# Optimization experiments

Hardware: AMD Instinct MI355X
Metric: run time of the kernel (lower is better)

## Reference

```python
import jax, jax.numpy as jnp
import numpy as np

SWIGLU_ALPHA = 1.702
SWIGLU_LIMIT = 7.0
TOP_K = 4


def setup_inputs() -> dict:
    key = jax.random.key(0)
    k = jax.random.split(key, 5)
    B, S, D, E, I = 2, 1024, 1024, 8, 2048
    return {
        "hidden_states": jax.random.normal(k[0], (B, S, D), dtype=jnp.float32),
        "router_weight": jax.random.normal(k[1], (E, D), dtype=jnp.float32) * 0.02,
        "router_bias": jnp.zeros((E,), dtype=jnp.float32),
        "gate_up_proj": jax.random.normal(k[2], (E, 2 * I, D), dtype=jnp.float32) * 0.02,
        "gate_up_proj_bias": jnp.zeros((E, 2 * I), dtype=jnp.float32),
        "down_proj": jax.random.normal(k[3], (E, D, I), dtype=jnp.float32) * 0.02,
        "down_proj_bias": jnp.zeros((E, D), dtype=jnp.float32),
    }


def reference(hidden_states, router_weight, router_bias, gate_up_proj,
              gate_up_proj_bias, down_proj, down_proj_bias):
    B, S, D = hidden_states.shape
    E = router_weight.shape[0]
    x = hidden_states.reshape(-1, D)                      # [N, D]
    N = x.shape[0]

    # --- router: top-k + post-softmax normalization (softmax in fp32) ---
    logits = x @ router_weight.T + router_bias            # [N, E]
    topk_logits, topk_idx = jax.lax.top_k(logits, TOP_K)  # [N, K]
    topk_w = jax.nn.softmax(topk_logits.astype(jnp.float32), axis=-1)

    # dense combine weights: zero for unselected experts (math-equivalent to
    # scatter -> grouped GEMM -> gather+weighted-sum in the torch code)
    combine = jnp.zeros((N, E), dtype=jnp.float32)
    combine = combine.at[jnp.arange(N)[:, None], topk_idx].set(topk_w)  # [N, E]

    # --- experts: clamped SwiGLU FFN, all experts on all tokens ---
    gate_up = jnp.einsum('nd,ejd->nej', x, gate_up_proj) + gate_up_proj_bias  # [N, E, 2I]
    gate, up = jnp.split(gate_up, 2, axis=-1)             # [N, E, I] each
    gate = jnp.minimum(gate, SWIGLU_LIMIT)
    up = jnp.clip(up, -SWIGLU_LIMIT, SWIGLU_LIMIT)
    act = (up + 1.0) * gate * jax.nn.sigmoid(SWIGLU_ALPHA * gate)  # [N, E, I]
    out = jnp.einsum('nei,edi->ned', act, down_proj) + down_proj_bias  # [N, E, D]

    # --- weighted combine over selected experts ---
    y = jnp.einsum('ned,ne->nd', out, combine.astype(out.dtype))  # [N, D]
    return y.reshape(B, S, D)
```

## Files before the change

kernel.cpp:

```cpp
#include <hip/hip_runtime.h>
#include <stdint.h>
#include <math.h>

#define NTOK   2048
#define DDIM   1024
#define ENUM   8
#define IDIM   2048
#define TWOI   4096
#define TOPKN  4
#define CAPROWS 10240

typedef unsigned short ushort_t;
typedef __attribute__((ext_vector_type(8))) short short8;
typedef __attribute__((ext_vector_type(4))) float f4;

#define VMCNT(n) asm volatile("s_waitcnt vmcnt(" #n ")" ::: "memory")
#define CFENCE() asm volatile("" ::: "memory")
#define BARRIER() do { CFENCE(); __builtin_amdgcn_s_barrier(); CFENCE(); } while (0)

__device__ inline ushort_t f2bf(float f) {
    union { float f; uint32_t u; } v; v.f = f;
    uint32_t u = v.u;
    u += 0x7FFFu + ((u >> 16) & 1u);
    return (ushort_t)(u >> 16);
}

__device__ inline void gload16(const ushort_t* g, ushort_t* l) {
    __builtin_amdgcn_global_load_lds(
        (const __attribute__((address_space(1))) uint32_t*)(uintptr_t)g,
        (__attribute__((address_space(3))) uint32_t*)(uint32_t)(uintptr_t)l,
        16, 0, 0);
}

__global__ void cvt_all_kernel(const float* __restrict__ gup, const float* __restrict__ dwn,
                               ushort_t* __restrict__ dst, int* __restrict__ meta) {
    if (blockIdx.x == 0 && threadIdx.x < 64) meta[threadIdx.x] = 0;
    const int n1 = ENUM * TWOI * DDIM / 8;
    const int n2 = ENUM * DDIM * IDIM / 8;
    int i = blockIdx.x * 256 + threadIdx.x;
    const float4* src;
    if (i < n1) src = (const float4*)gup + 2 * (size_t)i;
    else if (i < n1 + n2) src = (const float4*)dwn + 2 * (size_t)(i - n1);
    else return;
    float4 a = src[0], b = src[1];
    uint4 o;
    o.x = (uint32_t)f2bf(a.x) | ((uint32_t)f2bf(a.y) << 16);
    o.y = (uint32_t)f2bf(a.z) | ((uint32_t)f2bf(a.w) << 16);
    o.z = (uint32_t)f2bf(b.x) | ((uint32_t)f2bf(b.y) << 16);
    o.w = (uint32_t)f2bf(b.z) | ((uint32_t)f2bf(b.w) << 16);
    ((uint4*)dst)[i] = o;
}

__global__ void router_kernel(const float* __restrict__ x, const float* __restrict__ rw,
                              const float* __restrict__ rb, int* __restrict__ topk_idx,
                              float* __restrict__ topk_w, int* __restrict__ counts) {
    int n = (blockIdx.x * 256 + threadIdx.x) >> 6;
    int lane = threadIdx.x & 63;
    const float* xr = x + (size_t)n * DDIM;
    double p[ENUM];
#pragma unroll
    for (int e = 0; e < ENUM; ++e) p[e] = 0.0;
    for (int d0 = 0; d0 < DDIM; d0 += 64) {
        double xv = (double)xr[d0 + lane];
#pragma unroll
        for (int e = 0; e < ENUM; ++e) p[e] += xv * (double)rw[e * DDIM + d0 + lane];
    }
#pragma unroll
    for (int e = 0; e < ENUM; ++e) {
        double v = p[e];
#pragma unroll
        for (int off = 32; off > 0; off >>= 1) v += __shfl_xor(v, off, 64);
        p[e] = v + (double)rb[e];
    }
    if (lane == 0) {
        int id[TOPKN]; double lv[TOPKN]; unsigned used = 0;
#pragma unroll
        for (int k = 0; k < TOPKN; ++k) {
            double best = -INFINITY; int bi = 0;
            for (int e = 0; e < ENUM; ++e)
                if (!((used >> e) & 1u) && p[e] > best) { best = p[e]; bi = e; }
            used |= 1u << bi; id[k] = bi; lv[k] = best;
        }
        float lf[TOPKN]; float s = 0.f; float w[TOPKN];
#pragma unroll
        for (int k = 0; k < TOPKN; ++k) lf[k] = (float)lv[k];
#pragma unroll
        for (int k = 0; k < TOPKN; ++k) { w[k] = expf(lf[k] - lf[0]); s += w[k]; }
        float inv = 1.f / s;
#pragma unroll
        for (int k = 0; k < TOPKN; ++k) {
            topk_idx[n * TOPKN + k] = id[k];
            topk_w[n * TOPKN + k] = w[k] * inv;
            atomicAdd(&counts[id[k]], 1);
        }
    }
}

__global__ void assign_kernel(const int* __restrict__ topk_idx, const float* __restrict__ topk_w,
                              const int* __restrict__ counts, int* __restrict__ fill,
                              int* __restrict__ row_token, float* __restrict__ row_weight,
                              int* __restrict__ row_of_pair,
                              int* __restrict__ base, int* __restrict__ padcnt,
                              int* __restrict__ totalp) {
    int baseL[ENUM]; int run = 0;
#pragma unroll
    for (int e = 0; e < ENUM; ++e) {
        baseL[e] = run;
        run += (counts[e] + 255) & ~255;
    }
    int n = blockIdx.x * 256 + threadIdx.x;
    if (n == 0) {
#pragma unroll
        for (int e = 0; e < ENUM; ++e) {
            base[e] = baseL[e];
            padcnt[e] = (counts[e] + 255) & ~255;
        }
        *totalp = run;
    }
    if (n >= NTOK) return;
    for (int k = 0; k < TOPKN; ++k) {
        int e = topk_idx[n * TOPKN + k];
        int pos = atomicAdd(&fill[e], 1);
        int row = baseL[e] + pos;
        row_token[row] = n;
        row_weight[row] = topk_w[n * TOPKN + k];
        row_of_pair[n * TOPKN + k] = row;
    }
}

__global__ void gather_kernel(const float* __restrict__ x, const int* __restrict__ row_token,
                              const int* __restrict__ base, const int* __restrict__ counts,
                              const int* __restrict__ padcnt, const int* __restrict__ totalp,
                              ushort_t* __restrict__ A) {
    int r = blockIdx.x;
    if (r >= *totalp) return;
    int e = 0;
#pragma unroll
    for (int i = 0; i < ENUM; ++i) if (r >= base[i] + padcnt[i]) e = i + 1;
    bool valid = (r - base[e]) < counts[e];
    int t = threadIdx.x;
    float4 v = make_float4(0.f, 0.f, 0.f, 0.f);
    if (valid) {
        int n = row_token[r];
        v = ((const float4*)(x + (size_t)n * DDIM))[t];
    }
    ushort4 o; o.x = f2bf(v.x); o.y = f2bf(v.y); o.z = f2bf(v.z); o.w = f2bf(v.w);
    ((ushort4*)(A + (size_t)r * DDIM))[t] = o;
}

__global__ __launch_bounds__(512, 2)
void gemm1_kernel(const ushort_t* __restrict__ A, const ushort_t* __restrict__ Wg,
                  const float* __restrict__ gub, ushort_t* __restrict__ act,
                  const int* __restrict__ base, const int* __restrict__ padcnt) {
    const int e = blockIdx.z;
    const int mt = blockIdx.y;
    if (mt * 256 >= padcnt[e]) return;
    const int nt = blockIdx.x;
    const int row0 = base[e] + mt * 256;

    extern __shared__ char smem[];
    ushort_t* sA = (ushort_t*)smem;
    ushort_t* sG = (ushort_t*)(smem + 65536);
    ushort_t* sU = (ushort_t*)(smem + 98304);

    const int t = threadIdx.x;
    const int lane = t & 63;
    const int wid = t >> 6;
    const int wm = wid >> 2;
    const int wn = wid & 3;
    const int r15 = lane & 15, quad = lane >> 4;
    const int sw = r15 & 7;

    const int srow = t >> 3;
    const int sunit = (t & 7) ^ (srow & 7);
    const ushort_t* gA = A + (size_t)(row0 + srow) * DDIM + sunit * 8;
    const ushort_t* gG = Wg + ((size_t)e * TWOI + nt * 128 + srow) * DDIM + sunit * 8;
    const ushort_t* gU = gG + (size_t)IDIM * DDIM;

    f4 accg[8][2], accu[8][2];
    const f4 zero = {0.f, 0.f, 0.f, 0.f};
#pragma unroll
    for (int i = 0; i < 8; ++i)
#pragma unroll
        for (int j = 0; j < 2; ++j) { accg[i][j] = zero; accu[i][j] = zero; }

#define STG1A(ks, b) do {                                                    \
    const int k0_ = (ks) * 64;                                               \
    ushort_t* dA = sA + (b) * 16384 + t * 8;                                 \
    gload16(gA + k0_,                        dA);                            \
    gload16(gA + (size_t)64  * DDIM + k0_,   dA + 4096);                     \
    gload16(gA + (size_t)128 * DDIM + k0_,   dA + 8192);                     \
    gload16(gA + (size_t)192 * DDIM + k0_,   dA + 12288);                    \
} while (0)
#define STG1GU(ks, b) do {                                                   \
    const int k0_ = (ks) * 64;                                               \
    ushort_t* dG = sG + (b) * 8192  + t * 8;                                 \
    ushort_t* dU = sU + (b) * 8192  + t * 8;                                 \
    gload16(gG + k0_,                        dG);                            \
    gload16(gG + (size_t)64 * DDIM + k0_,    dG + 4096);                     \
    gload16(gU + k0_,                        dU);                            \
    gload16(gU + (size_t)64 * DDIM + k0_,    dU + 4096);                     \
} while (0)

    STG1A(0, 0); STG1GU(0, 0);
    const int NKS = DDIM / 64;
    for (int ks = 0; ks < NKS; ++ks) {
        const int cur = ks & 1;
        VMCNT(0);
        BARRIER();
        const ushort_t* bA = sA + cur * 16384;
        const ushort_t* bG = sG + cur * 8192;
        const ushort_t* bU = sU + cur * 8192;
        const bool pf = (ks + 1 < NKS);
#pragma unroll
        for (int kc = 0; kc < 2; ++kc) {
            const int uoff = ((kc * 4 + quad) ^ sw) * 8;
            short8 gF[2], uF[2];
#pragma unroll
            for (int j = 0; j < 2; ++j) {
                gF[j] = *(const short8*)(bG + (wn * 32 + j * 16 + r15) * 64 + uoff);
                uF[j] = *(const short8*)(bU + (wn * 32 + j * 16 + r15) * 64 + uoff);
            }
#pragma unroll
            for (int mh = 0; mh < 2; ++mh) {
                short8 aF[4];
#pragma unroll
                for (int i = 0; i < 4; ++i)
                    aF[i] = *(const short8*)(bA + (wm * 128 + (mh * 4 + i) * 16 + r15) * 64 + uoff);
                if (pf && mh == 0) {
                    if (kc == 0) STG1A(ks + 1, cur ^ 1);
                    else         STG1GU(ks + 1, cur ^ 1);
                }
                __builtin_amdgcn_sched_barrier(0);
                __builtin_amdgcn_s_setprio(1);
#pragma unroll
                for (int i = 0; i < 4; ++i)
#pragma unroll
                    for (int j = 0; j < 2; ++j) {
                        accg[mh * 4 + i][j] = __builtin_amdgcn_mfma_f32_16x16x32_bf16(aF[i], gF[j], accg[mh * 4 + i][j], 0, 0, 0);
                        accu[mh * 4 + i][j] = __builtin_amdgcn_mfma_f32_16x16x32_bf16(aF[i], uF[j], accu[mh * 4 + i][j], 0, 0, 0);
                    }
                __builtin_amdgcn_s_setprio(0);
                __builtin_amdgcn_sched_barrier(0);
            }
        }
    }
#undef STG1A
#undef STG1GU

    const int rowbase = row0 + wm * 128;
    const int col0 = nt * 128 + wn * 32;
#pragma unroll
    for (int j = 0; j < 2; ++j) {
        const int col = col0 + j * 16 + r15;
        const float bg = gub[e * TWOI + col];
        const float bu = gub[e * TWOI + IDIM + col];
#pragma unroll
        for (int mf = 0; mf < 8; ++mf) {
#pragma unroll
            for (int r = 0; r < 4; ++r) {
                const int row = rowbase + mf * 16 + quad * 4 + r;
                float g = fminf(accg[mf][j][r] + bg, 7.0f);
                float u = fminf(fmaxf(accu[mf][j][r] + bu, -7.0f), 7.0f);
                float a = (u + 1.0f) * g / (1.0f + __expf(-1.702f * g));
                act[(size_t)row * IDIM + col] = f2bf(a);
            }
        }
    }
}

__global__ __launch_bounds__(256, 2)
void gemm2_kernel(const ushort_t* __restrict__ A, const ushort_t* __restrict__ Wd,
                  const float* __restrict__ dwb, const float* __restrict__ row_weight,
                  float* __restrict__ contrib,
                  const int* __restrict__ base, const int* __restrict__ padcnt) {
    const int e = blockIdx.z;
    const int mt = blockIdx.y;
    if (mt * 128 >= padcnt[e]) return;
    const int nt = blockIdx.x;
    const int row0 = base[e] + mt * 128;

    extern __shared__ char smem[];
    ushort_t* sA = (ushort_t*)smem;
    ushort_t* sB = (ushort_t*)(smem + 32768);

    const int t = threadIdx.x;
    const int lane = t & 63;
    const int wid = t >> 6;
    const int wm = wid >> 1;
    const int wn = wid & 1;
    const int r15 = lane & 15, quad = lane >> 4;
    const int sw = r15 & 7;

    const int gr = t >> 3;
    const int gu = (t & 7) ^ (gr & 7);
    const ushort_t* gA = A + (size_t)(row0 + gr) * IDIM + gu * 8;
    const ushort_t* gB = Wd + ((size_t)e * DDIM + nt * 128 + gr) * IDIM + gu * 8;

    f4 acc[4][4];
    const f4 zero = {0.f, 0.f, 0.f, 0.f};
#pragma unroll
    for (int i = 0; i < 4; ++i)
#pragma unroll
        for (int j = 0; j < 4; ++j) acc[i][j] = zero;

#define STG2A(ks, b) do {                                                    \
    const int k0_ = (ks) * 64;                                               \
    ushort_t* dA = sA + (b) * 8192 + t * 8;                                  \
    gload16(gA + k0_,                       dA);                             \
    gload16(gA + (size_t)32 * IDIM + k0_,   dA + 2048);                      \
    gload16(gA + (size_t)64 * IDIM + k0_,   dA + 4096);                      \
    gload16(gA + (size_t)96 * IDIM + k0_,   dA + 6144);                      \
} while (0)
#define STG2B(ks, b) do {                                                    \
    const int k0_ = (ks) * 64;                                               \
    ushort_t* dB = sB + (b) * 8192 + t * 8;                                  \
    gload16(gB + k0_,                       dB);                             \
    gload16(gB + (size_t)32 * IDIM + k0_,   dB + 2048);                      \
    gload16(gB + (size_t)64 * IDIM + k0_,   dB + 4096);                      \
    gload16(gB + (size_t)96 * IDIM + k0_,   dB + 6144);                      \
} while (0)

    STG2A(0, 0); STG2B(0, 0);
    const int NKS = IDIM / 64;
    for (int ks = 0; ks < NKS; ++ks) {
        const int cur = ks & 1;
        VMCNT(0);
        BARRIER();
        const ushort_t* bA = sA + cur * 8192;
        const ushort_t* bB = sB + cur * 8192;
        const bool pf = (ks + 1 < NKS);
#pragma unroll
        for (int kc = 0; kc < 2; ++kc) {
            const int uoff = ((kc * 4 + quad) ^ sw) * 8;
            short8 aF[4], bF[4];
#pragma unroll
            for (int j = 0; j < 4; ++j)
                bF[j] = *(const short8*)(bB + (wn * 64 + j * 16 + r15) * 64 + uoff);
#pragma unroll
            for (int i = 0; i < 4; ++i)
                aF[i] = *(const short8*)(bA + (wm * 64 + i * 16 + r15) * 64 + uoff);
            if (pf) {
                if (kc == 0) STG2A(ks + 1, cur ^ 1);
                else         STG2B(ks + 1, cur ^ 1);
            }
            __builtin_amdgcn_sched_barrier(0);
            __builtin_amdgcn_s_setprio(1);
#pragma unroll
            for (int i = 0; i < 4; ++i)
#pragma unroll
                for (int j = 0; j < 4; ++j)
                    acc[i][j] = __builtin_amdgcn_mfma_f32_16x16x32_bf16(aF[i], bF[j], acc[i][j], 0, 0, 0);
            __builtin_amdgcn_s_setprio(0);
            __builtin_amdgcn_sched_barrier(0);
        }
    }
#undef STG2A
#undef STG2B

    const int rowbase = row0 + wm * 64;
    const int col0 = nt * 128 + wn * 64;
    float bs[4];
#pragma unroll
    for (int j = 0; j < 4; ++j) bs[j] = dwb[e * DDIM + col0 + j * 16 + r15];
#pragma unroll
    for (int mf = 0; mf < 4; ++mf) {
#pragma unroll
        for (int r = 0; r < 4; ++r) {
            const int row = rowbase + mf * 16 + quad * 4 + r;
            const float w = row_weight[row];
#pragma unroll
            for (int j = 0; j < 4; ++j) {
                const int col = col0 + j * 16 + r15;
                contrib[(size_t)row * DDIM + col] = (acc[mf][j][r] + bs[j]) * w;
            }
        }
    }
}

__global__ void combine_kernel(const float* __restrict__ contrib, const int* __restrict__ row_of_pair,
                               float* __restrict__ out) {
    int n = blockIdx.x;
    int t = threadIdx.x;
    int r0 = row_of_pair[n * 4 + 0], r1 = row_of_pair[n * 4 + 1];
    int r2 = row_of_pair[n * 4 + 2], r3 = row_of_pair[n * 4 + 3];
    float4 a = ((const float4*)(contrib + (size_t)r0 * DDIM))[t];
    float4 b = ((const float4*)(contrib + (size_t)r1 * DDIM))[t];
    float4 c = ((const float4*)(contrib + (size_t)r2 * DDIM))[t];
    float4 d = ((const float4*)(contrib + (size_t)r3 * DDIM))[t];
    float4 s;
    s.x = a.x + b.x + c.x + d.x;
    s.y = a.y + b.y + c.y + d.y;
    s.z = a.z + b.z + c.z + d.z;
    s.w = a.w + b.w + c.w + d.w;
    ((float4*)(out + (size_t)n * DDIM))[t] = s;
}

extern "C" void kernel_launch(void* const* d_in, const int* in_sizes, int n_in,
                              void* d_out, int out_size, void* d_ws, size_t ws_size,
                              hipStream_t stream) {
    const float* x   = (const float*)d_in[0];
    const float* rw  = (const float*)d_in[1];
    const float* rb  = (const float*)d_in[2];
    const float* gup = (const float*)d_in[3];
    const float* gub = (const float*)d_in[4];
    const float* dwn = (const float*)d_in[5];
    const float* dwb = (const float*)d_in[6];
    float* out = (float*)d_out;

    char* ws = (char*)d_ws;
    size_t off = 0;
    auto alloc = [&](size_t bytes) -> void* {
        void* p = ws + off;
        off += (bytes + 255) & ~(size_t)255;
        return p;
    };
    ushort_t* Wg   = (ushort_t*)alloc((size_t)ENUM * TWOI * DDIM * 2);
    ushort_t* Wd   = (ushort_t*)alloc((size_t)ENUM * DDIM * IDIM * 2);
    char* unionbuf = (char*)alloc((size_t)CAPROWS * DDIM * 4);
    ushort_t* Ar      = (ushort_t*)unionbuf;
    float*    CONTRIB = (float*)unionbuf;
    ushort_t* ACT  = (ushort_t*)alloc((size_t)CAPROWS * IDIM * 2);
    int*   topk_idx    = (int*)alloc(NTOK * 4 * 4);
    float* topk_w      = (float*)alloc(NTOK * 4 * 4);
    int*   row_of_pair = (int*)alloc(NTOK * 4 * 4);
    int*   row_token   = (int*)alloc(CAPROWS * 4);
    float* row_weight  = (float*)alloc(CAPROWS * 4);
    int*   meta        = (int*)alloc(256);
    int* counts = meta;      int* fill = meta + 8;
    int* base   = meta + 16; int* padcnt = meta + 24;
    int* totalp = meta + 32;

    const int ncvt8 = (ENUM * TWOI * DDIM + ENUM * DDIM * IDIM) / 8;

    cvt_all_kernel<<<(ncvt8 + 255) / 256, 256, 0, stream>>>(gup, dwn, Wg, meta);
    router_kernel<<<NTOK / 4, 256, 0, stream>>>(x, rw, rb, topk_idx, topk_w, counts);
    assign_kernel<<<NTOK / 256, 256, 0, stream>>>(topk_idx, topk_w, counts, fill,
                                                  row_token, row_weight, row_of_pair,
                                                  base, padcnt, totalp);
    gather_kernel<<<CAPROWS, 256, 0, stream>>>(x, row_token, base, counts, padcnt, totalp, Ar);
    gemm1_kernel<<<dim3(IDIM / 128, 8, ENUM), 512, 131072, stream>>>(Ar, Wg, gub, ACT, base, padcnt);
    gemm2_kernel<<<dim3(DDIM / 128, 16, ENUM), 256, 65536, stream>>>(ACT, Wd, dwb, row_weight, CONTRIB, base, padcnt);
    combine_kernel<<<NTOK, 256, 0, stream>>>(CONTRIB, row_of_pair, out);
}
```

Before: 562.1 us.

## Remap GEMM block indices for XCD-aware L2 locality and vectorize router loads

Both expert GEMMs now rebuild (expert, m-tile, n-tile) from a linearized block id. Blocks that share an A row-tile and are spread round-robin across the 8 XCDs are regrouped so each XCD works on the same m-tile across its n-tiles. The aim is better L2 reuse of the activation and weight tiles on MI355X's chiplet L2 caches. The router kernel also switches to float4 loads with an unrolled loop, which changes the order of the double-precision accumulation slightly.

```diff
diff --git a/kernel.cpp b/kernel.cpp
--- a/kernel.cpp
+++ b/kernel.cpp
@@ -56,14 +56,22 @@
                               float* __restrict__ topk_w, int* __restrict__ counts) {
     int n = (blockIdx.x * 256 + threadIdx.x) >> 6;
     int lane = threadIdx.x & 63;
-    const float* xr = x + (size_t)n * DDIM;
+    const float4* x4 = (const float4*)(x + (size_t)n * DDIM);
+    const float4* w4 = (const float4*)rw;
     double p[ENUM];
 #pragma unroll
     for (int e = 0; e < ENUM; ++e) p[e] = 0.0;
-    for (int d0 = 0; d0 < DDIM; d0 += 64) {
-        double xv = (double)xr[d0 + lane];
-#pragma unroll
-        for (int e = 0; e < ENUM; ++e) p[e] += xv * (double)rw[e * DDIM + d0 + lane];
+#pragma unroll
+    for (int c = 0; c < 4; ++c) {
+        float4 xv = x4[c * 64 + lane];
+#pragma unroll
+        for (int e = 0; e < ENUM; ++e) {
+            float4 wv = w4[e * (DDIM / 4) + c * 64 + lane];
+            p[e] += (double)xv.x * (double)wv.x;
+            p[e] += (double)xv.y * (double)wv.y;
+            p[e] += (double)xv.z * (double)wv.z;
+            p[e] += (double)xv.w * (double)wv.w;
+        }
     }
 #pragma unroll
     for (int e = 0; e < ENUM; ++e) {
@@ -152,10 +160,14 @@
 void gemm1_kernel(const ushort_t* __restrict__ A, const ushort_t* __restrict__ Wg,
                   const float* __restrict__ gub, ushort_t* __restrict__ act,
                   const int* __restrict__ base, const int* __restrict__ padcnt) {
-    const int e = blockIdx.z;
-    const int mt = blockIdx.y;
+    const int L = blockIdx.x + 16 * blockIdx.y + 128 * blockIdx.z;
+    const int xcd = L & 7;
+    const int s = L >> 3;
+    const int nt = s & 15;
+    const int grp = ((s >> 4) << 3) | xcd;
+    const int e = grp >> 3;
+    const int mt = grp & 7;
     if (mt * 256 >= padcnt[e]) return;
-    const int nt = blockIdx.x;
     const int row0 = base[e] + mt * 256;
 
     extern __shared__ char smem[];
@@ -274,10 +286,14 @@
                   const float* __restrict__ dwb, const float* __restrict__ row_weight,
                   float* __restrict__ contrib,
                   const int* __restrict__ base, const int* __restrict__ padcnt) {
-    const int e = blockIdx.z;
-    const int mt = blockIdx.y;
+    const int L = blockIdx.x + 8 * blockIdx.y + 128 * blockIdx.z;
+    const int xcd = L & 7;
+    const int s = L >> 3;
+    const int nt = s & 7;
+    const int grp = ((s >> 3) << 3) | xcd;
+    const int e = grp >> 4;
+    const int mt = grp & 15;
     if (mt * 128 >= padcnt[e]) return;
-    const int nt = blockIdx.x;
     const int row0 = base[e] + mt * 128;
 
     extern __shared__ char smem[];
```

Result: slower. 603.2 us (+7.3%).

## Enlarge gemm2 tile to 256 rows with 512 threads, spread gemm1 prefetch

Applied to the files above, without the earlier changes.

The down-projection GEMM now uses 256-row M tiles computed by 512 threads (8 waves), which doubles reuse of each loaded weight tile and halves the grid along M. The prefetch stages in both GEMMs are split into smaller chunks issued across more sub-iterations, so global loads interleave more evenly with MFMA work. The router loads x and weights as float4. The larger gemm2 tile uses 96KB of LDS per block, which may lower occupancy and add padding waste for experts whose row counts are not multiples of 256.

```diff
diff --git a/kernel.cpp b/kernel.cpp
--- a/kernel.cpp
+++ b/kernel.cpp
@@ -56,14 +56,22 @@
                               float* __restrict__ topk_w, int* __restrict__ counts) {
     int n = (blockIdx.x * 256 + threadIdx.x) >> 6;
     int lane = threadIdx.x & 63;
-    const float* xr = x + (size_t)n * DDIM;
+    const float4* x4 = (const float4*)(x + (size_t)n * DDIM);
+    const float4* w4 = (const float4*)rw;
     double p[ENUM];
 #pragma unroll
     for (int e = 0; e < ENUM; ++e) p[e] = 0.0;
-    for (int d0 = 0; d0 < DDIM; d0 += 64) {
-        double xv = (double)xr[d0 + lane];
-#pragma unroll
-        for (int e = 0; e < ENUM; ++e) p[e] += xv * (double)rw[e * DDIM + d0 + lane];
+#pragma unroll
+    for (int c = 0; c < 4; ++c) {
+        float4 xv = x4[c * 64 + lane];
+#pragma unroll
+        for (int e = 0; e < ENUM; ++e) {
+            float4 wv = w4[e * (DDIM / 4) + c * 64 + lane];
+            p[e] += (double)xv.x * (double)wv.x;
+            p[e] += (double)xv.y * (double)wv.y;
+            p[e] += (double)xv.z * (double)wv.z;
+            p[e] += (double)xv.w * (double)wv.w;
+        }
     }
 #pragma unroll
     for (int e = 0; e < ENUM; ++e) {
@@ -184,25 +192,32 @@
 #pragma unroll
         for (int j = 0; j < 2; ++j) { accg[i][j] = zero; accu[i][j] = zero; }
 
-#define STG1A(ks, b) do {                                                    \
+#define STG1A1(ks, b) do {                                                   \
     const int k0_ = (ks) * 64;                                               \
     ushort_t* dA = sA + (b) * 16384 + t * 8;                                 \
     gload16(gA + k0_,                        dA);                            \
     gload16(gA + (size_t)64  * DDIM + k0_,   dA + 4096);                     \
+} while (0)
+#define STG1A2(ks, b) do {                                                   \
+    const int k0_ = (ks) * 64;                                               \
+    ushort_t* dA = sA + (b) * 16384 + t * 8;                                 \
     gload16(gA + (size_t)128 * DDIM + k0_,   dA + 8192);                     \
     gload16(gA + (size_t)192 * DDIM + k0_,   dA + 12288);                    \
 } while (0)
-#define STG1GU(ks, b) do {                                                   \
+#define STG1G(ks, b) do {                                                    \
     const int k0_ = (ks) * 64;                                               \
     ushort_t* dG = sG + (b) * 8192  + t * 8;                                 \
-    ushort_t* dU = sU + (b) * 8192  + t * 8;                                 \
     gload16(gG + k0_,                        dG);                            \
     gload16(gG + (size_t)64 * DDIM + k0_,    dG + 4096);                     \
+} while (0)
+#define STG1U(ks, b) do {                                                    \
+    const int k0_ = (ks) * 64;                                               \
+    ushort_t* dU = sU + (b) * 8192  + t * 8;                                 \
     gload16(gU + k0_,                        dU);                            \
     gload16(gU + (size_t)64 * DDIM + k0_,    dU + 4096);                     \
 } while (0)
 
-    STG1A(0, 0); STG1GU(0, 0);
+    STG1A1(0, 0); STG1A2(0, 0); STG1G(0, 0); STG1U(0, 0);
     const int NKS = DDIM / 64;
     for (int ks = 0; ks < NKS; ++ks) {
         const int cur = ks & 1;
@@ -227,9 +242,9 @@
 #pragma unroll
                 for (int i = 0; i < 4; ++i)
                     aF[i] = *(const short8*)(bA + (wm * 128 + (mh * 4 + i) * 16 + r15) * 64 + uoff);
-                if (pf && mh == 0) {
-                    if (kc == 0) STG1A(ks + 1, cur ^ 1);
-                    else         STG1GU(ks + 1, cur ^ 1);
+                if (pf) {
+                    if (kc == 0) { if (mh == 0) STG1A1(ks + 1, cur ^ 1); else STG1A2(ks + 1, cur ^ 1); }
+                    else         { if (mh == 0) STG1G(ks + 1, cur ^ 1);  else STG1U(ks + 1, cur ^ 1); }
                 }
                 __builtin_amdgcn_sched_barrier(0);
                 __builtin_amdgcn_s_setprio(1);
@@ -245,8 +260,10 @@
             }
         }
     }
-#undef STG1A
-#undef STG1GU
+#undef STG1A1
+#undef STG1A2
+#undef STG1G
+#undef STG1U
 
     const int rowbase = row0 + wm * 128;
     const int col0 = nt * 128 + wn * 32;
@@ -269,20 +286,20 @@
     }
 }
 
-__global__ __launch_bounds__(256, 2)
+__global__ __launch_bounds__(512, 2)
 void gemm2_kernel(const ushort_t* __restrict__ A, const ushort_t* __restrict__ Wd,
                   const float* __restrict__ dwb, const float* __restrict__ row_weight,
                   float* __restrict__ contrib,
                   const int* __restrict__ base, const int* __restrict__ padcnt) {
     const int e = blockIdx.z;
     const int mt = blockIdx.y;
-    if (mt * 128 >= padcnt[e]) return;
+    if (mt * 256 >= padcnt[e]) return;
     const int nt = blockIdx.x;
-    const int row0 = base[e] + mt * 128;
+    const int row0 = base[e] + mt * 256;
 
     extern __shared__ char smem[];
     ushort_t* sA = (ushort_t*)smem;
-    ushort_t* sB = (ushort_t*)(smem + 32768);
+    ushort_t* sB = (ushort_t*)(smem + 65536);
 
     const int t = threadIdx.x;
     const int lane = t & 63;
@@ -292,10 +309,10 @@
     const int r15 = lane & 15, quad = lane >> 4;
     const int sw = r15 & 7;
 
-    const int gr = t >> 3;
-    const int gu = (t & 7) ^ (gr & 7);
-    const ushort_t* gA = A + (size_t)(row0 + gr) * IDIM + gu * 8;
-    const ushort_t* gB = Wd + ((size_t)e * DDIM + nt * 128 + gr) * IDIM + gu * 8;
+    const int srow = t >> 3;
+    const int sunit = (t & 7) ^ (srow & 7);
+    const ushort_t* gA = A + (size_t)(row0 + srow) * IDIM + sunit * 8;
+    const ushort_t* gB = Wd + ((size_t)e * DDIM + nt * 128 + srow) * IDIM + sunit * 8;
 
     f4 acc[4][4];
     const f4 zero = {0.f, 0.f, 0.f, 0.f};
@@ -304,30 +321,36 @@
 #pragma unroll
         for (int j = 0; j < 4; ++j) acc[i][j] = zero;
 
-#define STG2A(ks, b) do {                                                    \
-    const int k0_ = (ks) * 64;                                               \
-    ushort_t* dA = sA + (b) * 8192 + t * 8;                                  \
-    gload16(gA + k0_,                       dA);                             \
-    gload16(gA + (size_t)32 * IDIM + k0_,   dA + 2048);                      \
-    gload16(gA + (size_t)64 * IDIM + k0_,   dA + 4096);                      \
-    gload16(gA + (size_t)96 * IDIM + k0_,   dA + 6144);                      \
-} while (0)
-#define STG2B(ks, b) do {                                                    \
+#define STG2A1(ks, b) do {                                                   \
+    const int k0_ = (ks) * 64;                                               \
+    ushort_t* dA = sA + (b) * 16384 + t * 8;                                 \
+    gload16(gA + k0_,                        dA);                            \
+    gload16(gA + (size_t)64  * IDIM + k0_,   dA + 4096);                     \
+} while (0)
+#define STG2A2(ks, b) do {                                                   \
+    const int k0_ = (ks) * 64;                                               \
+    ushort_t* dA = sA + (b) * 16384 + t * 8;                                 \
+    gload16(gA + (size_t)128 * IDIM + k0_,   dA + 8192);                     \
+    gload16(gA + (size_t)192 * IDIM + k0_,   dA + 12288);                    \
+} while (0)
+#define STG2B1(ks, b) do {                                                   \
     const int k0_ = (ks) * 64;                                               \
     ushort_t* dB = sB + (b) * 8192 + t * 8;                                  \
-    gload16(gB + k0_,                       dB);                             \
-    gload16(gB + (size_t)32 * IDIM + k0_,   dB + 2048);                      \
-    gload16(gB + (size_t)64 * IDIM + k0_,   dB + 4096);                      \
-    gload16(gB + (size_t)96 * IDIM + k0_,   dB + 6144);                      \
-} while (0)
-
-    STG2A(0, 0); STG2B(0, 0);
+    gload16(gB + k0_,                        dB);                            \
+} while (0)
+#define STG2B2(ks, b) do {                                                   \
+    const int k0_ = (ks) * 64;                                               \
+    ushort_t* dB = sB + (b) * 8192 + t * 8;                                  \
+    gload16(gB + (size_t)64 * IDIM + k0_,    dB + 4096);                     \
+} while (0)
+
+    STG2A1(0, 0); STG2A2(0, 0); STG2B1(0, 0); STG2B2(0, 0);
     const int NKS = IDIM / 64;
     for (int ks = 0; ks < NKS; ++ks) {
         const int cur = ks & 1;
         VMCNT(0);
         BARRIER();
-        const ushort_t* bA = sA + cur * 8192;
+        const ushort_t* bA = sA + cur * 16384;
         const ushort_t* bB = sB + cur * 8192;
         const bool pf = (ks + 1 < NKS);
 #pragma unroll
@@ -341,8 +364,8 @@
             for (int i = 0; i < 4; ++i)
                 aF[i] = *(const short8*)(bA + (wm * 64 + i * 16 + r15) * 64 + uoff);
             if (pf) {
-                if (kc == 0) STG2A(ks + 1, cur ^ 1);
-                else         STG2B(ks + 1, cur ^ 1);
+                if (kc == 0) { STG2A1(ks + 1, cur ^ 1); STG2B1(ks + 1, cur ^ 1); }
+                else         { STG2A2(ks + 1, cur ^ 1); STG2B2(ks + 1, cur ^ 1); }
             }
             __builtin_amdgcn_sched_barrier(0);
             __builtin_amdgcn_s_setprio(1);
@@ -355,8 +378,10 @@
             __builtin_amdgcn_sched_barrier(0);
         }
     }
-#undef STG2A
-#undef STG2B
+#undef STG2A1
+#undef STG2A2
+#undef STG2B1
+#undef STG2B2
 
     const int rowbase = row0 + wm * 64;
     const int col0 = nt * 128 + wn * 64;
@@ -440,6 +465,6 @@
                                                   base, padcnt, totalp);
     gather_kernel<<<CAPROWS, 256, 0, stream>>>(x, row_token, base, counts, padcnt, totalp, Ar);
     gemm1_kernel<<<dim3(IDIM / 128, 8, ENUM), 512, 131072, stream>>>(Ar, Wg, gub, ACT, base, padcnt);
-    gemm2_kernel<<<dim3(DDIM / 128, 16, ENUM), 256, 65536, stream>>>(ACT, Wd, dwb, row_weight, CONTRIB, base, padcnt);
+    gemm2_kernel<<<dim3(DDIM / 128, 8, ENUM), 512, 98304, stream>>>(ACT, Wd, dwb, row_weight, CONTRIB, base, padcnt);
     combine_kernel<<<NTOK, 256, 0, stream>>>(CONTRIB, row_of_pair, out);
 }
```

Result: no change. 572.7 us (+1.9%).

## Deepen GEMM pipelines with BK=32 multi-stage buffers, enlarge gemm2 tiles

Applied to the files above, without the earlier changes.

Both grouped GEMMs drop from a double-buffered BK=64 K-loop to BK=32 stages with more buffers in flight: four buffers with three-ahead prefetch in gemm1, three with two-ahead in gemm2, and partial vmcnt waits instead of draining all loads each step. gemm2 moves to 512 threads and 256-row tiles with more shared memory. The router kernel loads x and weights as float4. The aim is to hide global-load latency behind MFMA work, at the cost of twice as many barriers per K and fewer resident blocks for the larger gemm2 tiles.

```diff
diff --git a/kernel.cpp b/kernel.cpp
--- a/kernel.cpp
+++ b/kernel.cpp
@@ -56,14 +56,22 @@
                               float* __restrict__ topk_w, int* __restrict__ counts) {
     int n = (blockIdx.x * 256 + threadIdx.x) >> 6;
     int lane = threadIdx.x & 63;
-    const float* xr = x + (size_t)n * DDIM;
+    const float4* x4 = (const float4*)(x + (size_t)n * DDIM);
+    const float4* w4 = (const float4*)rw;
     double p[ENUM];
 #pragma unroll
     for (int e = 0; e < ENUM; ++e) p[e] = 0.0;
-    for (int d0 = 0; d0 < DDIM; d0 += 64) {
-        double xv = (double)xr[d0 + lane];
-#pragma unroll
-        for (int e = 0; e < ENUM; ++e) p[e] += xv * (double)rw[e * DDIM + d0 + lane];
+#pragma unroll
+    for (int c = 0; c < 4; ++c) {
+        float4 xv = x4[c * 64 + lane];
+#pragma unroll
+        for (int e = 0; e < ENUM; ++e) {
+            float4 wv = w4[e * (DDIM / 4) + c * 64 + lane];
+            p[e] += (double)xv.x * (double)wv.x;
+            p[e] += (double)xv.y * (double)wv.y;
+            p[e] += (double)xv.z * (double)wv.z;
+            p[e] += (double)xv.w * (double)wv.w;
+        }
     }
 #pragma unroll
     for (int e = 0; e < ENUM; ++e) {
@@ -169,12 +177,12 @@
     const int wm = wid >> 2;
     const int wn = wid & 3;
     const int r15 = lane & 15, quad = lane >> 4;
-    const int sw = r15 & 7;
-
-    const int srow = t >> 3;
-    const int sunit = (t & 7) ^ (srow & 7);
-    const ushort_t* gA = A + (size_t)(row0 + srow) * DDIM + sunit * 8;
-    const ushort_t* gG = Wg + ((size_t)e * TWOI + nt * 128 + srow) * DDIM + sunit * 8;
+    const int uo = (quad ^ ((r15 >> 1) & 3)) * 8;
+
+    const int srow = t >> 2;
+    const int su = (t & 3) ^ ((t >> 3) & 3);
+    const ushort_t* gA = A + (size_t)(row0 + srow) * DDIM + su * 8;
+    const ushort_t* gG = Wg + ((size_t)e * TWOI + nt * 128 + srow) * DDIM + su * 8;
     const ushort_t* gU = gG + (size_t)IDIM * DDIM;
 
     f4 accg[8][2], accu[8][2];
@@ -185,64 +193,56 @@
         for (int j = 0; j < 2; ++j) { accg[i][j] = zero; accu[i][j] = zero; }
 
 #define STG1A(ks, b) do {                                                    \
-    const int k0_ = (ks) * 64;                                               \
-    ushort_t* dA = sA + (b) * 16384 + t * 8;                                 \
+    const int k0_ = (ks) * 32;                                               \
+    ushort_t* dA = sA + (b) * 8192 + t * 8;                                  \
     gload16(gA + k0_,                        dA);                            \
-    gload16(gA + (size_t)64  * DDIM + k0_,   dA + 4096);                     \
-    gload16(gA + (size_t)128 * DDIM + k0_,   dA + 8192);                     \
-    gload16(gA + (size_t)192 * DDIM + k0_,   dA + 12288);                    \
+    gload16(gA + (size_t)128 * DDIM + k0_,   dA + 4096);                     \
 } while (0)
 #define STG1GU(ks, b) do {                                                   \
-    const int k0_ = (ks) * 64;                                               \
-    ushort_t* dG = sG + (b) * 8192  + t * 8;                                 \
-    ushort_t* dU = sU + (b) * 8192  + t * 8;                                 \
-    gload16(gG + k0_,                        dG);                            \
-    gload16(gG + (size_t)64 * DDIM + k0_,    dG + 4096);                     \
-    gload16(gU + k0_,                        dU);                            \
-    gload16(gU + (size_t)64 * DDIM + k0_,    dU + 4096);                     \
+    const int k0_ = (ks) * 32;                                               \
+    gload16(gG + k0_,  sG + (b) * 4096 + t * 8);                             \
+    gload16(gU + k0_,  sU + (b) * 4096 + t * 8);                             \
 } while (0)
 
     STG1A(0, 0); STG1GU(0, 0);
-    const int NKS = DDIM / 64;
+    STG1A(1, 1); STG1GU(1, 1);
+    STG1A(2, 2); STG1GU(2, 2);
+    const int NKS = DDIM / 32;
     for (int ks = 0; ks < NKS; ++ks) {
-        const int cur = ks & 1;
-        VMCNT(0);
+        const int cur = ks & 3;
+        if (ks < NKS - 2)       VMCNT(8);
+        else if (ks == NKS - 2) VMCNT(4);
+        else                    VMCNT(0);
         BARRIER();
-        const ushort_t* bA = sA + cur * 16384;
-        const ushort_t* bG = sG + cur * 8192;
-        const ushort_t* bU = sU + cur * 8192;
-        const bool pf = (ks + 1 < NKS);
-#pragma unroll
-        for (int kc = 0; kc < 2; ++kc) {
-            const int uoff = ((kc * 4 + quad) ^ sw) * 8;
-            short8 gF[2], uF[2];
-#pragma unroll
-            for (int j = 0; j < 2; ++j) {
-                gF[j] = *(const short8*)(bG + (wn * 32 + j * 16 + r15) * 64 + uoff);
-                uF[j] = *(const short8*)(bU + (wn * 32 + j * 16 + r15) * 64 + uoff);
-            }
-#pragma unroll
-            for (int mh = 0; mh < 2; ++mh) {
-                short8 aF[4];
-#pragma unroll
-                for (int i = 0; i < 4; ++i)
-                    aF[i] = *(const short8*)(bA + (wm * 128 + (mh * 4 + i) * 16 + r15) * 64 + uoff);
-                if (pf && mh == 0) {
-                    if (kc == 0) STG1A(ks + 1, cur ^ 1);
-                    else         STG1GU(ks + 1, cur ^ 1);
+        const ushort_t* bA = sA + cur * 8192;
+        const ushort_t* bG = sG + cur * 4096;
+        const ushort_t* bU = sU + cur * 4096;
+        short8 gF[2], uF[2];
+#pragma unroll
+        for (int j = 0; j < 2; ++j) {
+            gF[j] = *(const short8*)(bG + (wn * 32 + j * 16 + r15) * 32 + uo);
+            uF[j] = *(const short8*)(bU + (wn * 32 + j * 16 + r15) * 32 + uo);
+        }
+        const bool pf = (ks + 3 < NKS);
+        const int nb = (ks + 3) & 3;
+#pragma unroll
+        for (int mh = 0; mh < 2; ++mh) {
+            short8 aF[4];
+#pragma unroll
+            for (int i = 0; i < 4; ++i)
+                aF[i] = *(const short8*)(bA + (wm * 128 + mh * 64 + i * 16 + r15) * 32 + uo);
+            if (pf) { if (mh == 0) STG1A(ks + 3, nb); else STG1GU(ks + 3, nb); }
+            __builtin_amdgcn_sched_barrier(0);
+            __builtin_amdgcn_s_setprio(1);
+#pragma unroll
+            for (int i = 0; i < 4; ++i)
+#pragma unroll
+                for (int j = 0; j < 2; ++j) {
+                    accg[mh * 4 + i][j] = __builtin_amdgcn_mfma_f32_16x16x32_bf16(aF[i], gF[j], accg[mh * 4 + i][j], 0, 0, 0);
+                    accu[mh * 4 + i][j] = __builtin_amdgcn_mfma_f32_16x16x32_bf16(aF[i], uF[j], accu[mh * 4 + i][j], 0, 0, 0);
                 }
-                __builtin_amdgcn_sched_barrier(0);
-                __builtin_amdgcn_s_setprio(1);
-#pragma unroll
-                for (int i = 0; i < 4; ++i)
-#pragma unroll
-                    for (int j = 0; j < 2; ++j) {
-                        accg[mh * 4 + i][j] = __builtin_amdgcn_mfma_f32_16x16x32_bf16(aF[i], gF[j], accg[mh * 4 + i][j], 0, 0, 0);
-                        accu[mh * 4 + i][j] = __builtin_amdgcn_mfma_f32_16x16x32_bf16(aF[i], uF[j], accu[mh * 4 + i][j], 0, 0, 0);
-                    }
-                __builtin_amdgcn_s_setprio(0);
-                __builtin_amdgcn_sched_barrier(0);
-            }
+            __builtin_amdgcn_s_setprio(0);
+            __builtin_amdgcn_sched_barrier(0);
         }
     }
 #undef STG1A
@@ -269,20 +269,20 @@
     }
 }
 
-__global__ __launch_bounds__(256, 2)
+__global__ __launch_bounds__(512, 4)
 void gemm2_kernel(const ushort_t* __restrict__ A, const ushort_t* __restrict__ Wd,
                   const float* __restrict__ dwb, const float* __restrict__ row_weight,
                   float* __restrict__ contrib,
                   const int* __restrict__ base, const int* __restrict__ padcnt) {
     const int e = blockIdx.z;
     const int mt = blockIdx.y;
-    if (mt * 128 >= padcnt[e]) return;
+    if (mt * 256 >= padcnt[e]) return;
     const int nt = blockIdx.x;
-    const int row0 = base[e] + mt * 128;
+    const int row0 = base[e] + mt * 256;
 
     extern __shared__ char smem[];
     ushort_t* sA = (ushort_t*)smem;
-    ushort_t* sB = (ushort_t*)(smem + 32768);
+    ushort_t* sB = (ushort_t*)(smem + 49152);
 
     const int t = threadIdx.x;
     const int lane = t & 63;
@@ -290,12 +290,12 @@
     const int wm = wid >> 1;
     const int wn = wid & 1;
     const int r15 = lane & 15, quad = lane >> 4;
-    const int sw = r15 & 7;
-
-    const int gr = t >> 3;
-    const int gu = (t & 7) ^ (gr & 7);
-    const ushort_t* gA = A + (size_t)(row0 + gr) * IDIM + gu * 8;
-    const ushort_t* gB = Wd + ((size_t)e * DDIM + nt * 128 + gr) * IDIM + gu * 8;
+    const int uo = (quad ^ ((r15 >> 1) & 3)) * 8;
+
+    const int srow = t >> 2;
+    const int su = (t & 3) ^ ((t >> 3) & 3);
+    const ushort_t* gA = A + (size_t)(row0 + srow) * IDIM + su * 8;
+    const ushort_t* gB = Wd + ((size_t)e * DDIM + nt * 128 + srow) * IDIM + su * 8;
 
     f4 acc[4][4];
     const f4 zero = {0.f, 0.f, 0.f, 0.f};
@@ -305,55 +305,47 @@
         for (int j = 0; j < 4; ++j) acc[i][j] = zero;
 
 #define STG2A(ks, b) do {                                                    \
-    const int k0_ = (ks) * 64;                                               \
+    const int k0_ = (ks) * 32;                                               \
     ushort_t* dA = sA + (b) * 8192 + t * 8;                                  \
-    gload16(gA + k0_,                       dA);                             \
-    gload16(gA + (size_t)32 * IDIM + k0_,   dA + 2048);                      \
-    gload16(gA + (size_t)64 * IDIM + k0_,   dA + 4096);                      \
-    gload16(gA + (size_t)96 * IDIM + k0_,   dA + 6144);                      \
+    gload16(gA + k0_,                        dA);                            \
+    gload16(gA + (size_t)128 * IDIM + k0_,   dA + 4096);                     \
 } while (0)
 #define STG2B(ks, b) do {                                                    \
-    const int k0_ = (ks) * 64;                                               \
-    ushort_t* dB = sB + (b) * 8192 + t * 8;                                  \
-    gload16(gB + k0_,                       dB);                             \
-    gload16(gB + (size_t)32 * IDIM + k0_,   dB + 2048);                      \
-    gload16(gB + (size_t)64 * IDIM + k0_,   dB + 4096);                      \
-    gload16(gB + (size_t)96 * IDIM + k0_,   dB + 6144);                      \
+    const int k0_ = (ks) * 32;                                               \
+    gload16(gB + k0_,  sB + (b) * 4096 + t * 8);                             \
 } while (0)
 
     STG2A(0, 0); STG2B(0, 0);
-    const int NKS = IDIM / 64;
+    STG2A(1, 1); STG2B(1, 1);
+    const int NKS = IDIM / 32;
+    int cur = 0;
     for (int ks = 0; ks < NKS; ++ks) {
-        const int cur = ks & 1;
-        VMCNT(0);
+        if (ks < NKS - 1) VMCNT(3);
+        else              VMCNT(0);
         BARRIER();
         const ushort_t* bA = sA + cur * 8192;
-        const ushort_t* bB = sB + cur * 8192;
-        const bool pf = (ks + 1 < NKS);
-#pragma unroll
-        for (int kc = 0; kc < 2; ++kc) {
-            const int uoff = ((kc * 4 + quad) ^ sw) * 8;
-            short8 aF[4], bF[4];
+        const ushort_t* bB = sB + cur * 4096;
+        short8 aF[4], bF[4];
+#pragma unroll
+        for (int j = 0; j < 4; ++j)
+            bF[j] = *(const short8*)(bB + (wn * 64 + j * 16 + r15) * 32 + uo);
+#pragma unroll
+        for (int i = 0; i < 4; ++i)
+            aF[i] = *(const short8*)(bA + (wm * 64 + i * 16 + r15) * 32 + uo);
+        if (ks + 2 < NKS) {
+            int nb = cur + 2; if (nb >= 3) nb -= 3;
+            STG2A(ks + 2, nb); STG2B(ks + 2, nb);
+        }
+        __builtin_amdgcn_sched_barrier(0);
+        __builtin_amdgcn_s_setprio(1);
+#pragma unroll
+        for (int i = 0; i < 4; ++i)
 #pragma unroll
             for (int j = 0; j < 4; ++j)
-                bF[j] = *(const short8*)(bB + (wn * 64 + j * 16 + r15) * 64 + uoff);
-#pragma unroll
-            for (int i = 0; i < 4; ++i)
-                aF[i] = *(const short8*)(bA + (wm * 64 + i * 16 + r15) * 64 + uoff);
-            if (pf) {
-                if (kc == 0) STG2A(ks + 1, cur ^ 1);
-                else         STG2B(ks + 1, cur ^ 1);
-            }
-            __builtin_amdgcn_sched_barrier(0);
-            __builtin_amdgcn_s_setprio(1);
-#pragma unroll
-            for (int i = 0; i < 4; ++i)
-#pragma unroll
-                for (int j = 0; j < 4; ++j)
-                    acc[i][j] = __builtin_amdgcn_mfma_f32_16x16x32_bf16(aF[i], bF[j], acc[i][j], 0, 0, 0);
-            __builtin_amdgcn_s_setprio(0);
-            __builtin_amdgcn_sched_barrier(0);
-        }
+                acc[i][j] = __builtin_amdgcn_mfma_f32_16x16x32_bf16(aF[i], bF[j], acc[i][j], 0, 0, 0);
+        __builtin_amdgcn_s_setprio(0);
+        __builtin_amdgcn_sched_barrier(0);
+        ++cur; if (cur == 3) cur = 0;
     }
 #undef STG2A
 #undef STG2B
@@ -440,6 +432,6 @@
                                                   base, padcnt, totalp);
     gather_kernel<<<CAPROWS, 256, 0, stream>>>(x, row_token, base, counts, padcnt, totalp, Ar);
     gemm1_kernel<<<dim3(IDIM / 128, 8, ENUM), 512, 131072, stream>>>(Ar, Wg, gub, ACT, base, padcnt);
-    gemm2_kernel<<<dim3(DDIM / 128, 16, ENUM), 256, 65536, stream>>>(ACT, Wd, dwb, row_weight, CONTRIB, base, padcnt);
+    gemm2_kernel<<<dim3(DDIM / 128, 8, ENUM), 512, 73728, stream>>>(ACT, Wd, dwb, row_weight, CONTRIB, base, padcnt);
     combine_kernel<<<NTOK, 256, 0, stream>>>(CONTRIB, row_of_pair, out);
 }
```

Result: no change. 562.5 us (+0.1%).
